# Kernel optimization log

Hardware: AMD Instinct MI355X
Metric: run time of the kernel (lower is better)

Reference implementation:

```python
import jax, jax.numpy as jnp
import numpy as np

B, N, D_MAX_LEN, D_LENGTH, D_MODEL, N_CLASS = 16, 1024, 512, 256, 128, 10
SAMPLE_K = 140  # factor(20) * ceil(ln(1024)) = 20*7; also n_top u (L_Q == L_K)


def setup_inputs() -> dict:
    key = jax.random.key(0)
    ks = jax.random.split(key, 10)
    s = 0.02
    return {
        "input_embedding": jax.random.normal(ks[0], (B, N, D_MAX_LEN), jnp.float32),
        "index_sample": jax.random.randint(ks[1], (N, SAMPLE_K), 0, N),
        # weights stored [in, out] (transpose of torch Linear.weight)
        "W_lin": jax.random.normal(ks[2], (D_MAX_LEN, D_LENGTH), jnp.float32) * s,
        "b_lin": jnp.zeros((D_LENGTH,), jnp.float32),
        "W_q": jax.random.normal(ks[3], (D_LENGTH, D_MODEL), jnp.float32) * s,
        "W_k": jax.random.normal(ks[4], (D_LENGTH, D_MODEL), jnp.float32) * s,
        "W_v": jax.random.normal(ks[5], (D_LENGTH, D_MODEL), jnp.float32) * s,
        "W_add": jax.random.normal(ks[6], (D_LENGTH, D_MODEL), jnp.float32) * s,
        "b_add": jnp.zeros((D_MODEL,), jnp.float32),
        "W_final": jax.random.normal(ks[7], (D_MODEL * N, N_CLASS), jnp.float32) * s,
        "b_final": jnp.zeros((N_CLASS,), jnp.float32),
    }


def reference(input_embedding, index_sample, W_lin, b_lin, W_q, W_k, W_v,
              W_add, b_add, W_final, b_final):
    # self.linear: [B, N, d_max_len] -> [B, N, d_length]
    x = input_embedding @ W_lin + b_lin
    b, n, _ = x.shape
    # single head (h=1): [B, 1, L, D]
    Q = (x @ W_q)[:, None]
    K = (x @ W_k)[:, None]
    V = (x @ W_v)[:, None]
    d = Q.shape[-1]
    L_K = n
    n_top = index_sample.shape[1]  # u == sample_k here

    # _prob_QK: gather sampled keys per query row, score against Q
    Kg = K[:, :, index_sample, :]                      # [B,1,L_Q,S,D]
    QK_sample = jnp.einsum('bhld,bhlsd->bhls', Q, Kg)  # [B,1,L_Q,S]
    M = QK_sample.max(-1) - QK_sample.sum(-1) / L_K    # sparsity measure
    _, M_top = jax.lax.top_k(M, n_top)                 # [B,1,u]

    Qr = jnp.take_along_axis(Q, M_top[..., None], axis=2)       # [B,1,u,D]
    scores = jnp.einsum('bhud,bhkd->bhuk', Qr, K) / np.sqrt(d)  # [B,1,u,L_K]

    # _get_initial_context (mask_flag=False): mean of V broadcast over L_Q
    ctx = jnp.broadcast_to(V.mean(axis=2, keepdims=True), V.shape)  # [B,1,L_Q,D]

    # _update_context: scatter softmax(scores) @ V into selected rows
    attn = jax.nn.softmax(scores, axis=-1)
    upd = jnp.einsum('bhuk,bhkd->bhud', attn, V)  # [B,1,u,D]
    bidx = jnp.arange(b)[:, None, None]
    hidx = jnp.arange(1)[None, :, None]
    ctx = ctx.at[bidx, hidx, M_top].set(upd)

    ctx = ctx[:, 0]                    # H=1 -> [B,N,D]
    out = ctx + (x @ W_add + b_add)    # residual add (dropout: eval mode)
    out = out.reshape(b, -1) @ W_final + b_final  # [B, n_class]
    return out
```

## Files before the change

### kernel.cpp

```cpp
#include <hip/hip_runtime.h>

typedef __attribute__((ext_vector_type(8))) short short8;
typedef __attribute__((ext_vector_type(4))) float f32x4;
typedef unsigned short u16;
typedef unsigned int u32;
typedef __attribute__((address_space(1))) const u32 gu32;
typedef __attribute__((address_space(3))) u32 lu32;

__device__ __forceinline__ u16 f2bf(float f){
  unsigned u = __float_as_uint(f);
  u += 0x7FFF + ((u >> 16) & 1);
  return (u16)(u >> 16);
}
__device__ __forceinline__ float bf2f(u16 h){ return __uint_as_float(((unsigned)h) << 16); }

#define BB   16
#define NN   1024
#define DML  512
#define DL   256
#define DM   128
#define NC   10
#define SK   140
#define KTOT (NN*DM)

__global__ void k_prep(const float* __restrict__ Wlin, const float* __restrict__ Wq,
                       const float* __restrict__ Wk, const float* __restrict__ Wv,
                       const float* __restrict__ Wadd,
                       u16* __restrict__ wlinT, u16* __restrict__ w4T,
                       const float* __restrict__ Wf, u16* __restrict__ wf2){
  int blk = blockIdx.x, t = threadIdx.x;
  if (blk < 512){
    int id = blk*256 + t;
    {
      int j = id >> 9;
      int k = id & 511;
      wlinT[id] = f2bf(Wlin[k*DL + j]);
    }
    {
      int j = id >> 8;
      int k = id & 255;
      const float* src = (j < 128) ? Wq : (j < 256) ? Wk : (j < 384) ? Wv : Wadd;
      int jj = j & 127;
      w4T[id] = f2bf(src[k*DM + jj]);
    }
  } else {
    int i4 = (blk-512)*256 + t;
    float4 v = ((const float4*)Wf)[i4];
    ushort4 o; o.x=f2bf(v.x); o.y=f2bf(v.y); o.z=f2bf(v.z); o.w=f2bf(v.w);
    ((ushort4*)wf2)[i4] = o;
  }
}

__device__ __forceinline__ void stage2(const u16* __restrict__ A, const u16* __restrict__ B,
                                       int K, int m0, int n0, int kb,
                                       u16* sA, u16* sB, int tid, int wave){
  #pragma unroll
  for (int i = 0; i < 4; ++i){
    int ci  = i*256 + tid;
    int row = ci >> 3;
    int kc  = (ci & 7) ^ (row & 7);
    __builtin_amdgcn_global_load_lds((gu32*)(A + (long)(m0+row)*K + kb + kc*8),
                                     (lu32*)(sA + (i*256 + wave*64)*8), 16, 0, 0);
    __builtin_amdgcn_global_load_lds((gu32*)(B + (long)(n0+row)*K + kb + kc*8),
                                     (lu32*)(sB + (i*256 + wave*64)*8), 16, 0, 0);
  }
}
__device__ __forceinline__ void compute64(const u16* sA, const u16* sB,
                                          int lane, int wrow, int wcol, f32x4 acc[4][4]){
  #pragma unroll
  for (int kk = 0; kk < 2; ++kk){
    short8 af[4], bfr[4];
    int cb = kk*4 + (lane >> 4);
    #pragma unroll
    for (int m_=0; m_<4; ++m_){
      int row = wrow + m_*16 + (lane & 15);
      af[m_] = *(const short8*)&sA[row*64 + ((cb ^ (row & 7)) << 3)];
    }
    #pragma unroll
    for (int n_=0; n_<4; ++n_){
      int row = wcol + n_*16 + (lane & 15);
      bfr[n_] = *(const short8*)&sB[row*64 + ((cb ^ (row & 7)) << 3)];
    }
    #pragma unroll
    for (int m_=0; m_<4; ++m_)
      #pragma unroll
      for (int n_=0; n_<4; ++n_)
        acc[m_][n_] = __builtin_amdgcn_mfma_f32_16x16x32_bf16(af[m_], bfr[n_], acc[m_][n_], 0, 0, 0);
  }
}
__device__ __forceinline__ void gemm_core_db(const u16* __restrict__ A, const u16* __restrict__ B,
                                             int K, int m0, int n0,
                                             u16* sA0, u16* sB0, u16* sA1, u16* sB1,
                                             f32x4 acc[4][4]){
  const int tid  = threadIdx.x;
  const int lane = tid & 63;
  const int wave = tid >> 6;
  const int wrow = (wave >> 1) * 64;
  const int wcol = (wave & 1) * 64;
  u16 *cA = sA0, *cB = sB0, *nA = sA1, *nB = sB1;
  stage2(A, B, K, m0, n0, 0, cA, cB, tid, wave);
  __syncthreads();
  int nt = K >> 6;
  for (int t = 0; t < nt-1; ++t){
    stage2(A, B, K, m0, n0, (t+1)*64, nA, nB, tid, wave);
    compute64(cA, cB, lane, wrow, wcol, acc);
    __syncthreads();
    u16* x;
    x = cA; cA = nA; nA = x;
    x = cB; cB = nB; nB = x;
  }
  compute64(cA, cB, lane, wrow, wcol, acc);
}

__global__ __launch_bounds__(256) void k_gemm_x(const float* __restrict__ A, const u16* __restrict__ B,
                                                const float* __restrict__ bias, u16* __restrict__ out){
  __shared__ u16 smem[12288];
  u16* sA = smem;
  u16* sB = smem + 4096;
  const int tid  = threadIdx.x;
  const int lane = tid & 63;
  const int wave = tid >> 6;
  const int wrow = (wave >> 1) * 32;
  const int wcol = (wave & 1) * 64;
  int m0 = blockIdx.x*64, n0 = blockIdx.y*128;
  f32x4 acc[2][4];
  f32x4 z = {0.f,0.f,0.f,0.f};
  #pragma unroll
  for (int m_=0;m_<2;++m_) for (int n_=0;n_<4;++n_) acc[m_][n_] = z;

  f32x4 ra[4];
  short8 rb[4];
  const int arow = tid >> 2, aq = tid & 3;

  {
    const float* src = A + (long)(m0+arow)*DML + aq*16;
    ra[0] = ((const f32x4*)src)[0]; ra[1] = ((const f32x4*)src)[1];
    ra[2] = ((const f32x4*)src)[2]; ra[3] = ((const f32x4*)src)[3];
    #pragma unroll
    for (int i=0;i<4;++i){
      int ci = i*256 + tid, row = ci>>3, kc = ci&7;
      rb[i] = *(const short8*)(B + (long)(n0+row)*DML + kc*8);
    }
  }
  {
    short8 o0, o1;
    #pragma unroll
    for (int j=0;j<4;++j){ o0[j]=(short)f2bf(ra[0][j]); o0[4+j]=(short)f2bf(ra[1][j]);
                           o1[j]=(short)f2bf(ra[2][j]); o1[4+j]=(short)f2bf(ra[3][j]); }
    int kc0 = aq*2, kc1 = aq*2+1;
    *(short8*)&sA[arow*64 + ((kc0 ^ (arow&7))<<3)] = o0;
    *(short8*)&sA[arow*64 + ((kc1 ^ (arow&7))<<3)] = o1;
    #pragma unroll
    for (int i=0;i<4;++i){
      int ci = i*256 + tid, row = ci>>3, kc = ci&7;
      *(short8*)&sB[row*64 + ((kc ^ (row&7))<<3)] = rb[i];
    }
  }
  __syncthreads();

  for (int tt = 0; tt < 8; ++tt){
    if (tt < 7){
      int kb = (tt+1)*64;
      const float* src = A + (long)(m0+arow)*DML + kb + aq*16;
      ra[0] = ((const f32x4*)src)[0]; ra[1] = ((const f32x4*)src)[1];
      ra[2] = ((const f32x4*)src)[2]; ra[3] = ((const f32x4*)src)[3];
      #pragma unroll
      for (int i=0;i<4;++i){
        int ci = i*256 + tid, row = ci>>3, kc = ci&7;
        rb[i] = *(const short8*)(B + (long)(n0+row)*DML + kb + kc*8);
      }
    }
    #pragma unroll
    for (int kk = 0; kk < 2; ++kk){
      short8 af[2], bfr[4];
      int cb = kk*4 + (lane >> 4);
      #pragma unroll
      for (int m_=0; m_<2; ++m_){
        int row = wrow + m_*16 + (lane & 15);
        af[m_] = *(const short8*)&sA[row*64 + ((cb ^ (row & 7)) << 3)];
      }
      #pragma unroll
      for (int n_=0; n_<4; ++n_){
        int row = wcol + n_*16 + (lane & 15);
        bfr[n_] = *(const short8*)&sB[row*64 + ((cb ^ (row & 7)) << 3)];
      }
      #pragma unroll
      for (int m_=0; m_<2; ++m_)
        #pragma unroll
        for (int n_=0; n_<4; ++n_)
          acc[m_][n_] = __builtin_amdgcn_mfma_f32_16x16x32_bf16(af[m_], bfr[n_], acc[m_][n_], 0, 0, 0);
    }
    __syncthreads();
    if (tt < 7){
      short8 o0, o1;
      #pragma unroll
      for (int j=0;j<4;++j){ o0[j]=(short)f2bf(ra[0][j]); o0[4+j]=(short)f2bf(ra[1][j]);
                             o1[j]=(short)f2bf(ra[2][j]); o1[4+j]=(short)f2bf(ra[3][j]); }
      int kc0 = aq*2, kc1 = aq*2+1;
      *(short8*)&sA[arow*64 + ((kc0 ^ (arow&7))<<3)] = o0;
      *(short8*)&sA[arow*64 + ((kc1 ^ (arow&7))<<3)] = o1;
      #pragma unroll
      for (int i=0;i<4;++i){
        int ci = i*256 + tid, row = ci>>3, kc = ci&7;
        *(short8*)&sB[row*64 + ((kc ^ (row&7))<<3)] = rb[i];
      }
      __syncthreads();
    }
  }

  u16* sC = sB;
  #pragma unroll
  for (int m_=0;m_<2;++m_)
    #pragma unroll
    for (int n_=0;n_<4;++n_)
      #pragma unroll
      for (int rr=0;rr<4;++rr){
        int row = wrow + m_*16 + (lane>>4)*4 + rr;
        int col = wcol + n_*16 + (lane & 15);
        sC[row*128 + col] = f2bf(acc[m_][n_][rr] + bias[n0 + col]);
      }
  __syncthreads();
  #pragma unroll
  for (int i = 0; i < 4; ++i){
    int ci = i*256 + tid;
    int row = ci >> 4, c = ci & 15;
    *(short8*)(out + (long)(m0+row)*DL + n0 + c*8) = *(const short8*)&sC[row*128 + c*8];
  }
}

__global__ __launch_bounds__(256) void k_gemm_qkva(const u16* __restrict__ A, const u16* __restrict__ B,
                                                   const float* __restrict__ badd,
                                                   u16* __restrict__ oq, u16* __restrict__ ok,
                                                   u16* __restrict__ ov, u16* __restrict__ oa){
  __shared__ u16 smem[32768];
  f32x4 acc[4][4];
  f32x4 z = {0.f,0.f,0.f,0.f};
  #pragma unroll
  for (int m_=0;m_<4;++m_) for (int n_=0;n_<4;++n_) acc[m_][n_] = z;
  int m0 = blockIdx.x*128;
  int tn = blockIdx.y;
  gemm_core_db(A, B, DL, m0, tn*128, smem, smem+8192, smem+16384, smem+24576, acc);
  int tid = threadIdx.x, lane = tid & 63, wave = tid >> 6;
  int wrow = (wave>>1)*64, wcol = (wave&1)*64;
  u16* dst = (tn==0) ? oq : (tn==1) ? ok : (tn==2) ? ov : oa;

  u16* sC = smem;
  #pragma unroll
  for (int m_=0;m_<4;++m_)
    #pragma unroll
    for (int n_=0;n_<4;++n_)
      #pragma unroll
      for (int r=0;r<4;++r){
        int row = wrow + m_*16 + (lane>>4)*4 + r;
        int col = wcol + n_*16 + (lane & 15);
        float v = acc[m_][n_][r];
        if (tn == 3) v += badd[col];
        sC[row*128 + col] = f2bf(v);
      }
  __syncthreads();
  u16* db = dst + (long)m0*DM;
  #pragma unroll
  for (int i = 0; i < 8; ++i){
    int ci = i*256 + tid;
    int row = ci >> 4, c = ci & 15;
    *(short8*)(db + (long)row*DM + c*8) = *(const short8*)&sC[row*128 + c*8];
  }
}

__global__ __launch_bounds__(256) void k_gemm_s(const u16* __restrict__ Q, const u16* __restrict__ Km,
                                                u16* __restrict__ S){
  __shared__ u16 smem[16384];
  u16* sA = smem;
  u16* sB = smem + 8192;
  const int tid = threadIdx.x, lane = tid & 63, wave = tid >> 6;
  const int wrow = (wave>>1)*64, wcol = (wave&1)*64;
  f32x4 acc[4][4];
  f32x4 z = {0.f,0.f,0.f,0.f};
  #pragma unroll
  for (int m_=0;m_<4;++m_) for (int n_=0;n_<4;++n_) acc[m_][n_] = z;
  int b = blockIdx.x, n0 = blockIdx.y*128, m0 = blockIdx.z*128;
  const u16* A = Q  + (long)b*NN*DM;
  const u16* B = Km + (long)b*NN*DM;

  stage2(A, B, DM, m0, n0, 0, sA, sB, tid, wave);
  __syncthreads();
  compute64(sA, sB, lane, wrow, wcol, acc);
  __syncthreads();
  stage2(A, B, DM, m0, n0, 64, sA, sB, tid, wave);
  __syncthreads();
  compute64(sA, sB, lane, wrow, wcol, acc);
  __syncthreads();

  u16* sS = smem;
  #pragma unroll
  for (int m_=0;m_<4;++m_)
    #pragma unroll
    for (int n_=0;n_<4;++n_)
      #pragma unroll
      for (int r=0;r<4;++r){
        int row = wrow + m_*16 + (lane>>4)*4 + r;
        int col = wcol + n_*16 + (lane & 15);
        sS[row*128 + col] = f2bf(acc[m_][n_][r]);
      }
  __syncthreads();

  u16* Sb = S + (long)b*NN*NN + (long)m0*NN + n0;
  #pragma unroll
  for (int i = 0; i < 8; ++i){
    int ci = i*256 + tid;
    int row = ci >> 4, c = ci & 15;
    *(short8*)(Sb + (long)row*NN + c*8) = *(const short8*)&sS[row*128 + c*8];
  }
}

__global__ void k_mscore(const u16* __restrict__ S, const int* __restrict__ idx, float* __restrict__ M){
  int b = blockIdx.x;
  int l = blockIdx.y*4 + (threadIdx.x >> 6);
  int lane = threadIdx.x & 63;
  const u16* Srow = S + (long)b*NN*NN + (long)l*NN;
  const int* ir = idx + l*SK;
  float mx = -1e30f, sm = 0.f;
  for (int s = lane; s < SK; s += 64){
    float v = bf2f(Srow[ir[s]]);
    mx = fmaxf(mx, v); sm += v;
  }
  #pragma unroll
  for (int o=32;o;o>>=1){ mx = fmaxf(mx, __shfl_xor(mx,o)); sm += __shfl_xor(sm,o); }
  if (lane == 0) M[b*NN + l] = mx - sm * (1.0f/1024.0f);
}

__global__ __launch_bounds__(256) void k_rankvm(const float* __restrict__ M, int* __restrict__ partial,
                                                const u16* __restrict__ V, float* __restrict__ vmean){
  __shared__ float sC[64];
  __shared__ float red[16][128];
  int blk = blockIdx.x, t = threadIdx.x;
  if (blk < 256){
    int jc = blk & 15, b = blk >> 4;
    const float* Mb = M + b*NN;
    if (t < 64) sC[t] = Mb[jc*64 + t];
    __syncthreads();
    int j0 = jc*64;
    float mi[4];
    int cnt[4] = {0,0,0,0};
    #pragma unroll
    for (int r=0;r<4;++r) mi[r] = Mb[t + r*256];
    for (int j = 0; j < 64; ++j){
      float mj = sC[j];
      int jg = j0 + j;
      #pragma unroll
      for (int r=0;r<4;++r){
        int i = t + r*256;
        cnt[r] += (mj > mi[r]) || (mj == mi[r] && jg < i);
      }
    }
    int* pb = partial + (b*16 + jc)*NN;
    #pragma unroll
    for (int r=0;r<4;++r) pb[t + r*256] = cnt[r];
  } else {
    int b = blk - 256;
    int d8 = t & 15, seg = t >> 4;
    const u16* Vb = V + (long)b*KTOT + seg*64*DM + d8*8;
    float acc[8] = {0,0,0,0,0,0,0,0};
    for (int l = 0; l < 64; ++l){
      short8 v = *(const short8*)(Vb + l*DM);
      #pragma unroll
      for (int j=0;j<8;++j) acc[j] += bf2f((u16)v[j]);
    }
    #pragma unroll
    for (int j=0;j<8;++j) red[seg][d8*8+j] = acc[j];
    __syncthreads();
    if (t < 128){
      float s = 0.f;
      #pragma unroll
      for (int g=0;g<16;++g) s += red[g][t];
      vmean[b*DM + t] = s * (1.0f/1024.0f);
    }
  }
}

__global__ __launch_bounds__(1024) void k_sel(const int* __restrict__ partial, int* __restrict__ mtop,
                                              int* __restrict__ selmap){
  int b = blockIdx.x, i = threadIdx.x;
  int cnt = 0;
  #pragma unroll
  for (int jc = 0; jc < 16; ++jc) cnt += partial[(b*16 + jc)*NN + i];
  selmap[b*NN + i] = (cnt < SK) ? cnt : -1;
  if (cnt < SK) mtop[b*SK + cnt] = i;
}

__global__ __launch_bounds__(256) void k_attn(const u16* __restrict__ S, const u16* __restrict__ V,
                                              const int* __restrict__ mtop, float* __restrict__ upd){
  __shared__ float sE[4][1024];
  __shared__ float redM[4][4];
  __shared__ float redS[4][4];
  __shared__ float sP[4][4][128];
  int b = blockIdx.x, u0 = blockIdx.y*4, t = threadIdx.x;
  int lane = t & 63, wave = t >> 6;
  const float inv = 0.08838834764831845f;

  int rows[4];
  #pragma unroll
  for (int r=0;r<4;++r) rows[r] = mtop[b*SK + u0 + r];

  float sv[4][4];
  float pm[4];
  const u16* Sb = S + (long)b*NN*NN;
  #pragma unroll
  for (int r=0;r<4;++r){
    ushort4 raw = ((const ushort4*)(Sb + (long)rows[r]*NN))[t];
    sv[r][0] = bf2f(raw.x)*inv; sv[r][1] = bf2f(raw.y)*inv;
    sv[r][2] = bf2f(raw.z)*inv; sv[r][3] = bf2f(raw.w)*inv;
    pm[r] = fmaxf(fmaxf(sv[r][0],sv[r][1]), fmaxf(sv[r][2],sv[r][3]));
  }
  #pragma unroll
  for (int o=32;o;o>>=1)
    #pragma unroll
    for (int r=0;r<4;++r) pm[r] = fmaxf(pm[r], __shfl_xor(pm[r],o));
  if (lane == 0){
    #pragma unroll
    for (int r=0;r<4;++r) redM[wave][r] = pm[r];
  }
  __syncthreads();
  float mx[4], ps[4];
  #pragma unroll
  for (int r=0;r<4;++r)
    mx[r] = fmaxf(fmaxf(redM[0][r],redM[1][r]), fmaxf(redM[2][r],redM[3][r]));
  #pragma unroll
  for (int r=0;r<4;++r){
    float s = 0.f;
    #pragma unroll
    for (int j=0;j<4;++j){
      float e = __expf(sv[r][j] - mx[r]);
      sE[r][t*4+j] = e;
      s += e;
    }
    ps[r] = s;
  }
  #pragma unroll
  for (int o=32;o;o>>=1)
    #pragma unroll
    for (int r=0;r<4;++r) ps[r] += __shfl_xor(ps[r],o);
  if (lane == 0){
    #pragma unroll
    for (int r=0;r<4;++r) redS[wave][r] = ps[r];
  }
  __syncthreads();
  float rZ[4];
  #pragma unroll
  for (int r=0;r<4;++r)
    rZ[r] = 1.0f / (redS[0][r]+redS[1][r]+redS[2][r]+redS[3][r]);

  int dg = t & 15;
  int kg = t >> 4;
  const u16* Vb = V + (long)b*KTOT + dg*8;
  float acc[4][8];
  #pragma unroll
  for (int r=0;r<4;++r)
    #pragma unroll
    for (int j=0;j<8;++j) acc[r][j] = 0.f;

  for (int k = kg; k < NN; k += 16){
    short8 v = *(const short8*)(Vb + (long)k*DM);
    float vf[8];
    #pragma unroll
    for (int j=0;j<8;++j) vf[j] = bf2f((u16)v[j]);
    #pragma unroll
    for (int r=0;r<4;++r){
      float e = sE[r][k];
      #pragma unroll
      for (int j=0;j<8;++j) acc[r][j] += e * vf[j];
    }
  }

  #pragma unroll
  for (int o=16;o<64;o<<=1)
    #pragma unroll
    for (int r=0;r<4;++r)
      #pragma unroll
      for (int j=0;j<8;++j) acc[r][j] += __shfl_xor(acc[r][j], o);

  if ((t & 63) < 16){
    #pragma unroll
    for (int r=0;r<4;++r)
      #pragma unroll
      for (int j=0;j<8;++j) sP[wave][r][dg*8+j] = acc[r][j];
  }
  __syncthreads();
  if (t < 128){
    #pragma unroll
    for (int r=0;r<4;++r){
      float s = sP[0][r][t] + sP[1][r][t] + sP[2][r][t] + sP[3][r][t];
      upd[((long)b*SK + u0 + r)*DM + t] = s * rZ[r];
    }
  }
}

__global__ __launch_bounds__(256) void k_final(const float* __restrict__ upd, const float* __restrict__ vmean,
                                               const int* __restrict__ selmap,
                                               const u16* __restrict__ Aad,
                                               const u16* __restrict__ wf2, float* __restrict__ part){
  int b = blockIdx.x, ch = blockIdx.y, t = threadIdx.x;
  long base = (long)b * KTOT;
  int k0 = ch * 4096;
  float acc[NC] = {0.f};
  for (int k = k0 + t; k < k0 + 4096; k += 256){
    int l = k >> 7, d = k & 127;
    int sel = selmap[b*NN + l];
    float c = (sel >= 0) ? upd[((long)b*SK + sel)*DM + d] : vmean[b*DM + d];
    float v = c + bf2f(Aad[base + k]);
    const u32* w32 = (const u32*)(wf2 + (long)k*NC);
    #pragma unroll
    for (int cc = 0; cc < 5; ++cc){
      u32 w = w32[cc];
      acc[2*cc]   += v * bf2f((u16)(w & 0xFFFF));
      acc[2*cc+1] += v * bf2f((u16)(w >> 16));
    }
  }
  __shared__ float lred[40];
  int lane = t & 63, wave = t >> 6;
  #pragma unroll
  for (int c = 0; c < NC; ++c){
    float v = acc[c];
    #pragma unroll
    for (int o=32;o;o>>=1) v += __shfl_xor(v,o);
    if (lane == 0) lred[wave*NC + c] = v;
  }
  __syncthreads();
  if (t < NC) part[(b*32 + ch)*NC + t] = lred[t] + lred[NC+t] + lred[2*NC+t] + lred[3*NC+t];
}

__global__ void k_out(const float* __restrict__ part, const float* __restrict__ bfin, float* __restrict__ out){
  int t = threadIdx.x;
  if (t < BB*NC){
    int b = t / NC, c = t % NC;
    float s = bfin[c];
    #pragma unroll
    for (int ch = 0; ch < 32; ++ch) s += part[(b*32 + ch)*NC + c];
    out[t] = s;
  }
}

extern "C" void kernel_launch(void* const* d_in, const int* in_sizes, int n_in,
                              void* d_out, int out_size, void* d_ws, size_t ws_size,
                              hipStream_t stream){
  const float* emb  = (const float*)d_in[0];
  const int*   idxs = (const int*)  d_in[1];
  const float* Wlin = (const float*)d_in[2];
  const float* blin = (const float*)d_in[3];
  const float* Wq   = (const float*)d_in[4];
  const float* Wk   = (const float*)d_in[5];
  const float* Wv   = (const float*)d_in[6];
  const float* Wadd = (const float*)d_in[7];
  const float* badd = (const float*)d_in[8];
  const float* Wfin = (const float*)d_in[9];
  const float* bfin = (const float*)d_in[10];
  float* out = (float*)d_out;

  char* p = (char*)d_ws;
  auto alloc = [&](size_t bytes)->char*{ char* r = p; p += (bytes + 255) & ~(size_t)255; return r; };
  u16*   wlinT  = (u16*)  alloc((size_t)DL*DML*2);
  u16*   w4T    = (u16*)  alloc((size_t)4*DM*DL*2);
  u16*   x_bf   = (u16*)  alloc((size_t)BB*NN*DL*2);
  u16*   q_bf   = (u16*)  alloc((size_t)BB*NN*DM*2);
  u16*   k_bf   = (u16*)  alloc((size_t)BB*NN*DM*2);
  u16*   v_bf   = (u16*)  alloc((size_t)BB*NN*DM*2);
  u16*   a_bf   = (u16*)  alloc((size_t)BB*NN*DM*2);
  u16*   s_bf   = (u16*)  alloc((size_t)BB*NN*NN*2);
  float* m_f    = (float*)alloc((size_t)BB*NN*4);
  int*   rankp  = (int*)  alloc((size_t)BB*16*NN*4);
  int*   mtop   = (int*)  alloc((size_t)BB*SK*4);
  int*   selmap = (int*)  alloc((size_t)BB*NN*4);
  float* vmean  = (float*)alloc((size_t)BB*DM*4);
  float* upd    = (float*)alloc((size_t)BB*SK*DM*4);
  u16*   wf2    = (u16*)  alloc((size_t)KTOT*NC*2);
  float* part   = (float*)alloc((size_t)BB*32*NC*4);

  k_prep<<<dim3(1792), dim3(256), 0, stream>>>(Wlin, Wq, Wk, Wv, Wadd, wlinT, w4T, Wfin, wf2);
  k_gemm_x<<<dim3(256, 2), dim3(256), 0, stream>>>(emb, wlinT, blin, x_bf);
  k_gemm_qkva<<<dim3(128, 4), dim3(256), 0, stream>>>(x_bf, w4T, badd, q_bf, k_bf, v_bf, a_bf);
  k_gemm_s<<<dim3(16, 8, 8), dim3(256), 0, stream>>>(q_bf, k_bf, s_bf);
  k_mscore<<<dim3(BB, NN/4), dim3(256), 0, stream>>>(s_bf, idxs, m_f);
  k_rankvm<<<dim3(272), dim3(256), 0, stream>>>(m_f, rankp, v_bf, vmean);
  k_sel<<<dim3(BB), dim3(1024), 0, stream>>>(rankp, mtop, selmap);
  k_attn<<<dim3(BB, SK/4), dim3(256), 0, stream>>>(s_bf, v_bf, mtop, upd);
  k_final<<<dim3(BB, 32), dim3(256), 0, stream>>>(upd, vmean, selmap, a_bf, wf2, part);
  k_out<<<dim3(1), dim3(256), 0, stream>>>(part, bfin, out);
}
```

Before: 104.6 us.

## Fuse sampled-score max/sum into QK GEMM epilogue, drop k_mscore kernel

The sparsity measure (max and sum over sampled keys) is now computed inside the S=QK^T GEMM epilogue from the tile already held in shared memory. Each block scans a padded u16 copy of index_sample, which k_prep builds in extra blocks, and writes per-column-tile partial max and sum. k_rankvm combines the 8 partials per row into M. This removes a separate kernel launch and its scattered global reads of S, at the cost of extra epilogue work and more partial-result traffic.

```diff
diff --git a/kernel.cpp b/kernel.cpp
--- a/kernel.cpp
+++ b/kernel.cpp
@@ -1,6 +1,7 @@
 #include <hip/hip_runtime.h>
 
 typedef __attribute__((ext_vector_type(8))) short short8;
+typedef __attribute__((ext_vector_type(8))) unsigned short ushort8;
 typedef __attribute__((ext_vector_type(4))) float f32x4;
 typedef unsigned short u16;
 typedef unsigned int u32;
@@ -27,7 +28,8 @@
                        const float* __restrict__ Wk, const float* __restrict__ Wv,
                        const float* __restrict__ Wadd,
                        u16* __restrict__ wlinT, u16* __restrict__ w4T,
-                       const float* __restrict__ Wf, u16* __restrict__ wf2){
+                       const float* __restrict__ Wf, u16* __restrict__ wf2,
+                       const int* __restrict__ idxs, u16* __restrict__ idxp){
   int blk = blockIdx.x, t = threadIdx.x;
   if (blk < 512){
     int id = blk*256 + t;
@@ -43,11 +45,16 @@
       int jj = j & 127;
       w4T[id] = f2bf(src[k*DM + jj]);
     }
-  } else {
+  } else if (blk < 1792){
     int i4 = (blk-512)*256 + t;
     float4 v = ((const float4*)Wf)[i4];
     ushort4 o; o.x=f2bf(v.x); o.y=f2bf(v.y); o.z=f2bf(v.z); o.w=f2bf(v.w);
     ((ushort4*)wf2)[i4] = o;
+  } else {
+    int id = (blk-1792)*256 + t;
+    int l = id / 144;
+    int s = id - l*144;
+    idxp[id] = (s < SK) ? (u16)idxs[l*SK + s] : (u16)0xFFFF;
   }
 }
 
@@ -268,7 +275,8 @@
 }
 
 __global__ __launch_bounds__(256) void k_gemm_s(const u16* __restrict__ Q, const u16* __restrict__ Km,
-                                                u16* __restrict__ S){
+                                                u16* __restrict__ S, const u16* __restrict__ idxp,
+                                                float* __restrict__ pmax, float* __restrict__ psum){
   __shared__ u16 smem[16384];
   u16* sA = smem;
   u16* sB = smem + 8192;
@@ -311,41 +319,56 @@
     int row = ci >> 4, c = ci & 15;
     *(short8*)(Sb + (long)row*NN + c*8) = *(const short8*)&sS[row*128 + c*8];
   }
-}
-
-__global__ void k_mscore(const u16* __restrict__ S, const int* __restrict__ idx, float* __restrict__ M){
-  int b = blockIdx.x;
-  int l = blockIdx.y*4 + (threadIdx.x >> 6);
-  int lane = threadIdx.x & 63;
-  const u16* Srow = S + (long)b*NN*NN + (long)l*NN;
-  const int* ir = idx + l*SK;
+
+  int l = tid >> 1, h = tid & 1;
+  const u16* ip = idxp + (long)(m0+l)*144 + h*72;
   float mx = -1e30f, sm = 0.f;
-  for (int s = lane; s < SK; s += 64){
-    float v = bf2f(Srow[ir[s]]);
-    mx = fmaxf(mx, v); sm += v;
-  }
-  #pragma unroll
-  for (int o=32;o;o>>=1){ mx = fmaxf(mx, __shfl_xor(mx,o)); sm += __shfl_xor(sm,o); }
-  if (lane == 0) M[b*NN + l] = mx - sm * (1.0f/1024.0f);
-}
-
-__global__ __launch_bounds__(256) void k_rankvm(const float* __restrict__ M, int* __restrict__ partial,
+  #pragma unroll
+  for (int j = 0; j < 9; ++j){
+    ushort8 v = *(const ushort8*)(ip + j*8);
+    #pragma unroll
+    for (int e = 0; e < 8; ++e){
+      int d = (int)v[e] - n0;
+      if ((unsigned)d < 128u){
+        float s = bf2f(sS[l*128 + d]);
+        mx = fmaxf(mx, s); sm += s;
+      }
+    }
+  }
+  float mo = __shfl_xor(mx, 1), so = __shfl_xor(sm, 1);
+  mx = fmaxf(mx, mo); sm += so;
+  if (h == 0){
+    int o = (b*8 + blockIdx.y)*NN + m0 + l;
+    pmax[o] = mx; psum[o] = sm;
+  }
+}
+
+__global__ __launch_bounds__(256) void k_rankvm(const float* __restrict__ pmax, const float* __restrict__ psum,
+                                                int* __restrict__ partial,
                                                 const u16* __restrict__ V, float* __restrict__ vmean){
-  __shared__ float sC[64];
-  __shared__ float red[16][128];
   int blk = blockIdx.x, t = threadIdx.x;
   if (blk < 256){
-    int jc = blk & 15, b = blk >> 4;
-    const float* Mb = M + b*NN;
-    if (t < 64) sC[t] = Mb[jc*64 + t];
+    __shared__ float Ml[1024];
+    int b = blk >> 4, jc = blk & 15;
+    #pragma unroll
+    for (int r=0;r<4;++r){
+      int i = t + r*256;
+      float mx = -1e30f, sm = 0.f;
+      #pragma unroll
+      for (int nb=0;nb<8;++nb){
+        mx = fmaxf(mx, pmax[(b*8+nb)*NN + i]);
+        sm += psum[(b*8+nb)*NN + i];
+      }
+      Ml[i] = mx - sm * (1.0f/1024.0f);
+    }
     __syncthreads();
-    int j0 = jc*64;
     float mi[4];
     int cnt[4] = {0,0,0,0};
     #pragma unroll
-    for (int r=0;r<4;++r) mi[r] = Mb[t + r*256];
+    for (int r=0;r<4;++r) mi[r] = Ml[t + r*256];
+    int j0 = jc*64;
     for (int j = 0; j < 64; ++j){
-      float mj = sC[j];
+      float mj = Ml[j0 + j];
       int jg = j0 + j;
       #pragma unroll
       for (int r=0;r<4;++r){
@@ -357,6 +380,7 @@
     #pragma unroll
     for (int r=0;r<4;++r) pb[t + r*256] = cnt[r];
   } else {
+    __shared__ float red[16][128];
     int b = blk - 256;
     int d8 = t & 15, seg = t >> 4;
     const u16* Vb = V + (long)b*KTOT + seg*64*DM + d8*8;
@@ -566,7 +590,9 @@
   u16*   v_bf   = (u16*)  alloc((size_t)BB*NN*DM*2);
   u16*   a_bf   = (u16*)  alloc((size_t)BB*NN*DM*2);
   u16*   s_bf   = (u16*)  alloc((size_t)BB*NN*NN*2);
-  float* m_f    = (float*)alloc((size_t)BB*NN*4);
+  u16*   idxp   = (u16*)  alloc((size_t)NN*144*2);
+  float* pmax   = (float*)alloc((size_t)BB*8*NN*4);
+  float* psum   = (float*)alloc((size_t)BB*8*NN*4);
   int*   rankp  = (int*)  alloc((size_t)BB*16*NN*4);
   int*   mtop   = (int*)  alloc((size_t)BB*SK*4);
   int*   selmap = (int*)  alloc((size_t)BB*NN*4);
@@ -575,12 +601,11 @@
   u16*   wf2    = (u16*)  alloc((size_t)KTOT*NC*2);
   float* part   = (float*)alloc((size_t)BB*32*NC*4);
 
-  k_prep<<<dim3(1792), dim3(256), 0, stream>>>(Wlin, Wq, Wk, Wv, Wadd, wlinT, w4T, Wfin, wf2);
+  k_prep<<<dim3(2368), dim3(256), 0, stream>>>(Wlin, Wq, Wk, Wv, Wadd, wlinT, w4T, Wfin, wf2, idxs, idxp);
   k_gemm_x<<<dim3(256, 2), dim3(256), 0, stream>>>(emb, wlinT, blin, x_bf);
   k_gemm_qkva<<<dim3(128, 4), dim3(256), 0, stream>>>(x_bf, w4T, badd, q_bf, k_bf, v_bf, a_bf);
-  k_gemm_s<<<dim3(16, 8, 8), dim3(256), 0, stream>>>(q_bf, k_bf, s_bf);
-  k_mscore<<<dim3(BB, NN/4), dim3(256), 0, stream>>>(s_bf, idxs, m_f);
-  k_rankvm<<<dim3(272), dim3(256), 0, stream>>>(m_f, rankp, v_bf, vmean);
+  k_gemm_s<<<dim3(16, 8, 8), dim3(256), 0, stream>>>(q_bf, k_bf, s_bf, idxp, pmax, psum);
+  k_rankvm<<<dim3(272), dim3(256), 0, stream>>>(pmax, psum, rankp, v_bf, vmean);
   k_sel<<<dim3(BB), dim3(1024), 0, stream>>>(rankp, mtop, selmap);
   k_attn<<<dim3(BB, SK/4), dim3(256), 0, stream>>>(s_bf, v_bf, mtop, upd);
   k_final<<<dim3(BB, 32), dim3(256), 0, stream>>>(upd, vmean, selmap, a_bf, wf2, part);
```

After: 104.8 us. Within noise of the previous version (+0.2%).
